# Kernel optimization log

Hardware: AMD Instinct MI355X
Metric: run time of the kernel (lower is better)

The kernel has to match this reference:

```python
import jax, jax.numpy as jnp
import numpy as np

DIM = 1024
N_HEADS = 16
HEAD_DIM = DIM // N_HEADS
HIDDEN = 4096  # round_up(4*DIM, 256)
ROPE_THETA = 10000.0
EPS = 1e-6


def setup_inputs() -> dict:
    key = jax.random.key(0)
    ks = jax.random.split(key, 10)
    s = 0.02
    return {
        "x": jax.random.normal(ks[0], (1, 4096, DIM), dtype=jnp.float32),
        "wq": jax.random.normal(ks[1], (DIM, DIM), dtype=jnp.float32) * s,
        "wk": jax.random.normal(ks[2], (DIM, DIM), dtype=jnp.float32) * s,
        "wv": jax.random.normal(ks[3], (DIM, DIM), dtype=jnp.float32) * s,
        "wo": jax.random.normal(ks[4], (DIM, DIM), dtype=jnp.float32) * s,
        "w1": jax.random.normal(ks[5], (HIDDEN, DIM), dtype=jnp.float32) * s,
        "w2": jax.random.normal(ks[6], (DIM, HIDDEN), dtype=jnp.float32) * s,
        "w3": jax.random.normal(ks[7], (HIDDEN, DIM), dtype=jnp.float32) * s,
        "g_attn": jnp.ones((DIM,), dtype=jnp.float32),
        "g_ffn": jnp.ones((DIM,), dtype=jnp.float32),
    }


def _rmsnorm(x, g):
    return x * jax.lax.rsqrt(jnp.mean(x * x, axis=-1, keepdims=True) + EPS) * g


def _rope_tables(seqlen):
    inv = 1.0 / (ROPE_THETA ** (jnp.arange(0, HEAD_DIM, 2, dtype=jnp.float32) / HEAD_DIM))
    ang = jnp.arange(seqlen, dtype=jnp.float32)[:, None] * inv[None, :]  # [s, hd/2]
    return jnp.cos(ang), jnp.sin(ang)


def _apply_rope(q, cos, sin):
    # q: [b, s, h, hd]; pairs (even, odd) treated as complex (re, im)
    b, s, h, d = q.shape
    qr = q.reshape(b, s, h, d // 2, 2)
    re, im = qr[..., 0], qr[..., 1]
    c = cos[None, :, None, :]
    sn = sin[None, :, None, :]
    out = jnp.stack([re * c - im * sn, re * sn + im * c], axis=-1)
    return out.reshape(b, s, h, d)


def reference(x, wq, wk, wv, wo, w1, w2, w3, g_attn, g_ffn):
    b, s, _ = x.shape
    xn = _rmsnorm(x, g_attn)
    q = (xn @ wq.T).reshape(b, s, N_HEADS, HEAD_DIM)
    k = (xn @ wk.T).reshape(b, s, N_HEADS, HEAD_DIM)
    v = (xn @ wv.T).reshape(b, s, N_HEADS, HEAD_DIM)
    cos, sin = _rope_tables(s)
    q = _apply_rope(q, cos, sin)
    k = _apply_rope(k, cos, sin)
    scores = jnp.einsum("bthd,bThd->bhtT", q, k) / np.sqrt(HEAD_DIM).astype(np.float32)
    probs = jax.nn.softmax(scores, axis=-1)
    attn = jnp.einsum("bhtT,bThd->bthd", probs, v).reshape(b, s, DIM)
    h = x + attn @ wo.T
    hn = _rmsnorm(h, g_ffn)
    ff = (jax.nn.silu(hn @ w1.T) * (hn @ w3.T)) @ w2.T
    return h + ff
```

## Files before the change

kernel.cpp:

```cpp
#include <hip/hip_runtime.h>

#define S_LEN 4096
#define DIMM  1024
#define NH    16
#define HD    64
#define HID   4096

typedef unsigned short u16;
typedef __attribute__((ext_vector_type(8))) short bf16x8;
typedef __attribute__((ext_vector_type(4))) short short4b;
typedef __attribute__((ext_vector_type(8))) unsigned short u16x8;
typedef __attribute__((ext_vector_type(4))) float f32x4;

__device__ __forceinline__ u16 f2bf(float f) {
  unsigned u = __float_as_uint(f);
  u += 0x7fffu + ((u >> 16) & 1u);
  return (u16)(u >> 16);
}
__device__ __forceinline__ float bf2f(u16 h) {
  return __uint_as_float(((unsigned)h) << 16);
}
__device__ __forceinline__ unsigned pack_bf16(float hi, float lo) {
  return __builtin_amdgcn_perm(__float_as_uint(hi), __float_as_uint(lo), 0x07060302u);
}
__device__ __forceinline__ float fexp2(float x) { return __builtin_amdgcn_exp2f(x); }

__device__ __forceinline__ void gl_lds16(const void* g, void* l) {
  __builtin_amdgcn_global_load_lds(
      (const __attribute__((address_space(1))) void*)g,
      (__attribute__((address_space(3))) void*)l, 16, 0, 0);
}

__global__ __launch_bounds__(256) void prep_kernel(
    const float* __restrict__ wq, const float* __restrict__ wk, const float* __restrict__ wv,
    const float* __restrict__ wo, const float* __restrict__ w1, const float* __restrict__ w3,
    const float* __restrict__ w2, const float* __restrict__ x, const float* __restrict__ g_attn,
    u16* __restrict__ wqkb, u16* __restrict__ wvb, u16* __restrict__ wob,
    u16* __restrict__ w13b, u16* __restrict__ w2b, u16* __restrict__ xnb,
    float* __restrict__ cosT, float* __restrict__ sinT) {
  int b = blockIdx.x;
  int t = threadIdx.x;
  if (b < 8192) {
    const float* src;
    u16* dst;
    int i;
    if (b < 2048) {
      int which = b >> 9, lb = b & 511;
      src = which == 0 ? wq : which == 1 ? wk : which == 2 ? wv : wo;
      dst = which == 0 ? wqkb : which == 1 ? (wqkb + (1 << 20)) : which == 2 ? wvb : wob;
      i = (lb * 256 + t) * 8;
    } else {
      int b2 = b - 2048, which = b2 >> 11, lb = b2 & 2047;
      src = which == 0 ? w1 : which == 1 ? w3 : w2;
      dst = which == 0 ? w13b : which == 1 ? (w13b + (4 << 20)) : w2b;
      i = (lb * 256 + t) * 8;
    }
    float4 a = *(const float4*)(src + i);
    float4 c = *(const float4*)(src + i + 4);
    u16x8 r;
    r[0] = f2bf(a.x); r[1] = f2bf(a.y); r[2] = f2bf(a.z); r[3] = f2bf(a.w);
    r[4] = f2bf(c.x); r[5] = f2bf(c.y); r[6] = f2bf(c.z); r[7] = f2bf(c.w);
    *(u16x8*)(dst + i) = r;
  } else if (b < 8704) {
    int idx = (b - 8192) * 256 + t;
    int pos = idx >> 5, i = idx & 31;
    double inv = pow(10000.0, -(double)(2 * i) / 64.0);
    double a = (double)pos * inv;
    cosT[idx] = (float)cos(a);
    sinT[idx] = (float)sin(a);
  } else {
    int row = b - 8704;
    const float4 v = *(const float4*)(x + (size_t)row * DIMM + t * 4);
    float ss = v.x * v.x + v.y * v.y + v.z * v.z + v.w * v.w;
#pragma unroll
    for (int off = 32; off > 0; off >>= 1) ss += __shfl_down(ss, off);
    __shared__ float red[4];
    if ((t & 63) == 0) red[t >> 6] = ss;
    __syncthreads();
    float tot = red[0] + red[1] + red[2] + red[3];
    float sc = rsqrtf(tot * (1.0f / DIMM) + 1e-6f);
    const float4 gv = *(const float4*)(g_attn + t * 4);
    ushort4 o;
    o.x = f2bf(v.x * sc * gv.x);
    o.y = f2bf(v.y * sc * gv.y);
    o.z = f2bf(v.z * sc * gv.z);
    o.w = f2bf(v.w * sc * gv.w);
    *(ushort4*)(xnb + (size_t)row * DIMM + t * 4) = o;
  }
}

__global__ __launch_bounds__(256) void rmsnorm_kernel(const float* __restrict__ x, const float* __restrict__ g,
                                                      u16* __restrict__ out) {
  int row = blockIdx.x;
  int t = threadIdx.x;
  const float4 v = *(const float4*)(x + (size_t)row * DIMM + t * 4);
  float ss = v.x * v.x + v.y * v.y + v.z * v.z + v.w * v.w;
#pragma unroll
  for (int off = 32; off > 0; off >>= 1) ss += __shfl_down(ss, off);
  __shared__ float red[4];
  if ((t & 63) == 0) red[t >> 6] = ss;
  __syncthreads();
  float tot = red[0] + red[1] + red[2] + red[3];
  float sc = rsqrtf(tot * (1.0f / DIMM) + 1e-6f);
  const float4 gv = *(const float4*)(g + t * 4);
  ushort4 o;
  o.x = f2bf(v.x * sc * gv.x);
  o.y = f2bf(v.y * sc * gv.y);
  o.z = f2bf(v.z * sc * gv.z);
  o.w = f2bf(v.w * sc * gv.w);
  *(ushort4*)(out + (size_t)row * DIMM + t * 4) = o;
}

template <int OUTMODE>
__global__ __launch_bounds__(512) void gemm_kernel(const u16* __restrict__ A, const u16* __restrict__ B,
                                                   void* Cout, const float* res, int N, int K, int lda,
                                                   int ldb, const float* cosT, const float* sinT) {
  __shared__ uint4 As0[1024], Bs0[1024], As1[1024], Bs1[1024];
  const int t = threadIdx.x;
  const int w = t >> 6, l = t & 63;
  const int wm = w >> 1, wn = w & 1;
  const int bm = blockIdx.y, bn = blockIdx.x;
  const int quad = l >> 4, lc = l & 15;

  f32x4 acc[2][4];
  const f32x4 zero = {0.0f, 0.0f, 0.0f, 0.0f};
#pragma unroll
  for (int mi = 0; mi < 2; mi++)
#pragma unroll
    for (int ni = 0; ni < 4; ni++) acc[mi][ni] = zero;

  const int band0 = t >> 6, kq0 = (t >> 4) & 3, row0 = t & 15;
  const u16* Ap0 = A + (size_t)(bm * 128 + band0 * 16 + row0) * lda + kq0 * 8;
  const u16* Bp0 = B + (size_t)(bn * 128 + band0 * 16 + row0) * ldb + kq0 * 8;
  if constexpr (OUTMODE == 4) {
    Ap0 += (size_t)blockIdx.z * K;
    Bp0 += (size_t)blockIdx.z * K;
  }
  const int abase = wm * 128 + l;
  const int bbase = wn * 256 + l;

#define STAGEL(AD, BD, K0)                 \
  do {                                     \
    gl_lds16(Ap0 + (K0), &(AD)[t]);        \
    gl_lds16(Ap0 + (K0) + 32, &(AD)[t + 512]); \
    gl_lds16(Bp0 + (K0), &(BD)[t]);        \
    gl_lds16(Bp0 + (K0) + 32, &(BD)[t + 512]); \
  } while (0)

#define COMPL(AS, BS)                                                                               \
  do {                                                                                              \
    _Pragma("unroll") for (int ks = 0; ks < 2; ks++) {                                              \
      bf16x8 af[2], bfr[4];                                                                         \
      _Pragma("unroll") for (int mi = 0; mi < 2; mi++)                                              \
          af[mi] = *(const bf16x8*)&(AS)[ks * 512 + abase + mi * 64];                               \
      _Pragma("unroll") for (int ni = 0; ni < 4; ni++)                                              \
          bfr[ni] = *(const bf16x8*)&(BS)[ks * 512 + bbase + ni * 64];                              \
      _Pragma("unroll") for (int mi = 0; mi < 2; mi++)                                              \
          _Pragma("unroll") for (int ni = 0; ni < 4; ni++)                                          \
              acc[mi][ni] = __builtin_amdgcn_mfma_f32_16x16x32_bf16(af[mi], bfr[ni], acc[mi][ni], 0, 0, 0); \
    }                                                                                               \
  } while (0)

  STAGEL(As0, Bs0, 0);
  __syncthreads();
  int k0 = 0;
  for (; k0 + 128 < K; k0 += 128) {
    STAGEL(As1, Bs1, k0 + 64);
    COMPL(As0, Bs0);
    __syncthreads();
    STAGEL(As0, Bs0, k0 + 128);
    COMPL(As1, Bs1);
    __syncthreads();
  }
  STAGEL(As1, Bs1, k0 + 64);
  COMPL(As0, Bs0);
  __syncthreads();
  COMPL(As1, Bs1);
#undef STAGEL
#undef COMPL

  const int rbase = bm * 128 + wm * 32 + quad * 4;
  const int cbase = bn * 128 + wn * 64 + lc;
  const float qs = (OUTMODE == 3 && bn < 8) ? 0.18033688011112f : 1.0f;
#pragma unroll
  for (int mi = 0; mi < 2; mi++) {
#pragma unroll
    for (int r = 0; r < 4; r++) {
      int row = rbase + mi * 16 + r;
#pragma unroll
      for (int ni = 0; ni < 4; ni++) {
        int col = cbase + ni * 16;
        if constexpr (OUTMODE == 0) {
          ((u16*)Cout)[(size_t)row * N + col] = f2bf(acc[mi][ni][r]);
        } else if constexpr (OUTMODE == 1) {
          size_t idx = (size_t)row * N + col;
          ((float*)Cout)[idx] = res[idx] + acc[mi][ni][r];
        } else if constexpr (OUTMODE == 2) {
          int h = row >> 6, din = row & 63;
          int kb = col >> 6, k63 = col & 63;
          int off = ((h << 6) + kb) * 4096 + (((din >> 4) << 1) + (k63 >> 5)) * 512 +
                    ((((k63 >> 2) & 3) << 4) + (din & 15)) * 8 + ((k63 >> 4) & 1) * 4 + (k63 & 3);
          ((u16*)Cout)[off] = f2bf(acc[mi][ni][r]);
        } else if constexpr (OUTMODE == 4) {
          size_t idx = (size_t)row * N + col;
          atomicAdd((float*)Cout + idx, acc[mi][ni][r]);
        } else {
          float v = acc[mi][ni][r];
          float pv = __shfl_xor(v, 1);
          int i = ((ni * 16 + lc) & 63) >> 1;
          float c = cosT[(row << 5) + i], s = sinT[(row << 5) + i];
          float o = (lc & 1) ? (pv * s + v * c) : (v * c - pv * s);
          ((u16*)Cout)[(size_t)row * N + col] = f2bf(o * qs);
        }
      }
    }
  }
}

__global__ __launch_bounds__(512) void gemm256_kernel(const u16* __restrict__ A, const u16* __restrict__ B,
                                                      u16* __restrict__ Cout, int N, int K, int lda) {
  __shared__ uint4 As0[1024], Bs0[1024], As1[1024], Bs1[1024], As2[1024], Bs2[1024];
  const int t = threadIdx.x;
  const int w = t >> 6, l = t & 63;
  const int wm = w >> 2, wn = w & 3;
  const int bm = blockIdx.y, bn = blockIdx.x;
  const int quad = l >> 4, lc = l & 15;

  f32x4 acc[8][4];
  const f32x4 zero = {0.0f, 0.0f, 0.0f, 0.0f};
#pragma unroll
  for (int mi = 0; mi < 8; mi++)
#pragma unroll
    for (int ni = 0; ni < 4; ni++) acc[mi][ni] = zero;

  const int band0 = t >> 6, kq0 = (t >> 4) & 3, row0 = t & 15;
  const u16* Ap0 = A + (size_t)(bm * 256 + band0 * 16 + row0) * lda + kq0 * 8;
  const u16* Bp0 = B + (size_t)(bn * 256 + band0 * 16 + row0) * K + kq0 * 8;
  const size_t Astep = (size_t)128 * lda;
  const size_t Bstep = (size_t)128 * K;

#define STG(AD, BD, K0)                           \
  do {                                            \
    gl_lds16(Ap0 + (K0), &(AD)[t]);               \
    gl_lds16(Ap0 + Astep + (K0), &(AD)[t + 512]); \
    gl_lds16(Bp0 + (K0), &(BD)[t]);               \
    gl_lds16(Bp0 + Bstep + (K0), &(BD)[t + 512]); \
  } while (0)

  const int NT = K >> 5;

#define PHASE(CA, CB, SA, SB, TT)                                              \
  do {                                                                         \
    if ((TT) + 2 < NT) STG(SA, SB, ((TT) + 2) * 32);                           \
    bf16x8 af[8], bfr[4];                                                      \
    _Pragma("unroll") for (int mi = 0; mi < 8; mi++)                           \
        af[mi] = *(const bf16x8*)&(CA)[(wm * 8 + mi) * 64 + l];                \
    _Pragma("unroll") for (int ni = 0; ni < 4; ni++)                           \
        bfr[ni] = *(const bf16x8*)&(CB)[(wn * 4 + ni) * 64 + l];               \
    __builtin_amdgcn_s_setprio(1);                                             \
    _Pragma("unroll") for (int mi = 0; mi < 8; mi++)                           \
        _Pragma("unroll") for (int ni = 0; ni < 4; ni++)                       \
            acc[mi][ni] = __builtin_amdgcn_mfma_f32_16x16x32_bf16(af[mi], bfr[ni], acc[mi][ni], 0, 0, 0); \
    __builtin_amdgcn_s_setprio(0);                                             \
    if ((TT) + 1 < NT) {                                                       \
      asm volatile("s_waitcnt lgkmcnt(0)" ::: "memory");                       \
      if ((TT) + 2 < NT) {                                                     \
        asm volatile("s_waitcnt vmcnt(4)" ::: "memory");                       \
      } else {                                                                 \
        asm volatile("s_waitcnt vmcnt(0)" ::: "memory");                       \
      }                                                                        \
      __builtin_amdgcn_s_barrier();                                            \
    }                                                                          \
  } while (0)

  STG(As0, Bs0, 0);
  STG(As1, Bs1, 32);
  asm volatile("s_waitcnt vmcnt(4)" ::: "memory");
  __builtin_amdgcn_s_barrier();

  for (int tt = 0; tt < NT; tt += 3) {
    PHASE(As0, Bs0, As2, Bs2, tt);
    if (tt + 1 < NT) PHASE(As1, Bs1, As0, Bs0, tt + 1);
    if (tt + 2 < NT) PHASE(As2, Bs2, As1, Bs1, tt + 2);
  }
#undef STG
#undef PHASE

  const int rbase = bm * 256 + wm * 128 + quad * 4;
  const int cbase = bn * 256 + wn * 64 + lc;
#pragma unroll
  for (int mi = 0; mi < 8; mi++) {
#pragma unroll
    for (int r = 0; r < 4; r++) {
      int row = rbase + mi * 16 + r;
#pragma unroll
      for (int ni = 0; ni < 4; ni++) {
        int col = cbase + ni * 16;
        Cout[(size_t)row * N + col] = f2bf(acc[mi][ni][r]);
      }
    }
  }
}

__global__ __launch_bounds__(512) void attn_kernel(const u16* __restrict__ Qm, const u16* __restrict__ Km,
                                                   const u16* __restrict__ Vsw, u16* __restrict__ Om) {
  __shared__ char smem[32768];
  uint4* Ks0 = (uint4*)smem;
  uint4* Vs0 = (uint4*)(smem + 8192);
  uint4* Ks1 = (uint4*)(smem + 16384);
  uint4* Vs1 = (uint4*)(smem + 24576);
  const int t = threadIdx.x;
  const int w = t >> 6, l = t & 63;
  const int quad = l >> 4, lc = l & 15;
  const int hd = blockIdx.y;
  const int qrow = blockIdx.x * 128 + w * 16;

  bf16x8 qf_[2];
#pragma unroll
  for (int ch = 0; ch < 2; ch++)
    qf_[ch] = *(const bf16x8*)(Qm + (size_t)(qrow + lc) * 2048 + hd * HD + ch * 32 + quad * 8);

  const f32x4 zero = {0.0f, 0.0f, 0.0f, 0.0f};
  const bf16x8 ones8 = {(short)0x3F80, (short)0x3F80, (short)0x3F80, (short)0x3F80,
                        (short)0x3F80, (short)0x3F80, (short)0x3F80, (short)0x3F80};
  f32x4 Oa[4];
#pragma unroll
  for (int df = 0; df < 4; df++) Oa[df] = zero;
  f32x4 lsacc = zero;

  const int s0 = t >> 7, c0 = (t >> 6) & 1, kq0 = (t >> 4) & 3, row0 = t & 15;
  const u16* Kp0 = Km + (size_t)(s0 * 16 + row0) * 2048 + hd * HD + c0 * 32 + kq0 * 8;
  const u16* Vp = Vsw + (size_t)(hd * HD) * 4096 + t * 8;

#define STAGEKV(KD, VD, TT)                                  \
  do {                                                       \
    gl_lds16(Kp0 + (size_t)(TT)*131072, &(KD)[t]);           \
    gl_lds16(Vp + (size_t)(TT)*4096, &(VD)[t]);              \
  } while (0)

#define TILE_COMPUTE(KS, VS)                                                                 \
  do {                                                                                       \
    f32x4 Sf[4];                                                                             \
    _Pragma("unroll") for (int kf = 0; kf < 4; kf++) {                                       \
      bf16x8 ka = *(const bf16x8*)&(KS)[kf * 128 + l];                                       \
      bf16x8 kb2 = *(const bf16x8*)&(KS)[kf * 128 + 64 + l];                                 \
      f32x4 z = __builtin_amdgcn_mfma_f32_16x16x32_bf16(ka, qf_[0], zero, 0, 0, 0);          \
      z = __builtin_amdgcn_mfma_f32_16x16x32_bf16(kb2, qf_[1], z, 0, 0, 0);                  \
      Sf[kf] = z;                                                                            \
    }                                                                                        \
    _Pragma("unroll") for (int kf = 0; kf < 4; kf++)                                         \
        _Pragma("unroll") for (int r = 0; r < 4; r++)                                        \
      Sf[kf][r] = fexp2(Sf[kf][r]);                                                          \
    union { bf16x8 v8; uint2 u2[2]; } p0, p1;                                                \
    p0.u2[0].x = pack_bf16(Sf[0][1], Sf[0][0]);                                              \
    p0.u2[0].y = pack_bf16(Sf[0][3], Sf[0][2]);                                              \
    p0.u2[1].x = pack_bf16(Sf[1][1], Sf[1][0]);                                              \
    p0.u2[1].y = pack_bf16(Sf[1][3], Sf[1][2]);                                              \
    p1.u2[0].x = pack_bf16(Sf[2][1], Sf[2][0]);                                              \
    p1.u2[0].y = pack_bf16(Sf[2][3], Sf[2][2]);                                              \
    p1.u2[1].x = pack_bf16(Sf[3][1], Sf[3][0]);                                              \
    p1.u2[1].y = pack_bf16(Sf[3][3], Sf[3][2]);                                              \
    lsacc = __builtin_amdgcn_mfma_f32_16x16x32_bf16(ones8, p0.v8, lsacc, 0, 0, 0);           \
    lsacc = __builtin_amdgcn_mfma_f32_16x16x32_bf16(ones8, p1.v8, lsacc, 0, 0, 0);           \
    _Pragma("unroll") for (int df = 0; df < 4; df++) {                                       \
      bf16x8 va = *(const bf16x8*)&(VS)[(df * 2) * 64 + l];                                  \
      bf16x8 vb = *(const bf16x8*)&(VS)[(df * 2 + 1) * 64 + l];                              \
      Oa[df] = __builtin_amdgcn_mfma_f32_16x16x32_bf16(va, p0.v8, Oa[df], 0, 0, 0);          \
      Oa[df] = __builtin_amdgcn_mfma_f32_16x16x32_bf16(vb, p1.v8, Oa[df], 0, 0, 0);          \
    }                                                                                        \
  } while (0)

  STAGEKV(Ks0, Vs0, 0);
  __syncthreads();

  for (int tt = 0; tt < 64; tt += 2) {
    STAGEKV(Ks1, Vs1, tt + 1);
    TILE_COMPUTE(Ks0, Vs0);
    __syncthreads();
    if (tt + 2 < 64) STAGEKV(Ks0, Vs0, tt + 2);
    TILE_COMPUTE(Ks1, Vs1);
    __syncthreads();
  }
#undef STAGEKV
#undef TILE_COMPUTE

  u16* ep = (u16*)smem;
  float invl = 1.0f / lsacc[0];
#pragma unroll
  for (int df = 0; df < 4; df++) {
    int qb = w * 16 + lc;
    int d = df * 16 + quad * 4;
    uint2 pv;
    pv.x = pack_bf16(Oa[df][1] * invl, Oa[df][0] * invl);
    pv.y = pack_bf16(Oa[df][3] * invl, Oa[df][2] * invl);
    *(uint2*)(ep + qb * 72 + d) = pv;
  }
  __syncthreads();
#pragma unroll
  for (int it = 0; it < 2; it++) {
    int qb = it * 64 + (t >> 3);
    int dp = (t & 7) * 8;
    u16x8 rowv = *(const u16x8*)(ep + qb * 72 + dp);
    *(u16x8*)(Om + (size_t)(blockIdx.x * 128 + qb) * DIMM + hd * HD + dp) = rowv;
  }
}

__global__ __launch_bounds__(256) void silu_mul_kernel(u16* __restrict__ u13) {
  int i = (blockIdx.x * 256 + threadIdx.x) * 8;
  int r = i >> 12, c = i & 4095;
  u16* up = u13 + (size_t)r * 8192 + c;
  u16x8 uv = *(const u16x8*)up;
  u16x8 gv = *(const u16x8*)(up + 4096);
  u16x8 o;
#pragma unroll
  for (int j = 0; j < 8; j++) {
    float a = bf2f(uv[j]);
    float b = bf2f(gv[j]);
    float sv = a / (1.0f + __expf(-a));
    o[j] = f2bf(sv * b);
  }
  *(u16x8*)up = o;
}

extern "C" void kernel_launch(void* const* d_in, const int* in_sizes, int n_in,
                              void* d_out, int out_size, void* d_ws, size_t ws_size,
                              hipStream_t stream) {
  const float* x      = (const float*)d_in[0];
  const float* wq     = (const float*)d_in[1];
  const float* wk     = (const float*)d_in[2];
  const float* wv     = (const float*)d_in[3];
  const float* wo     = (const float*)d_in[4];
  const float* w1     = (const float*)d_in[5];
  const float* w2     = (const float*)d_in[6];
  const float* w3     = (const float*)d_in[7];
  const float* g_attn = (const float*)d_in[8];
  const float* g_ffn  = (const float*)d_in[9];
  float* out = (float*)d_out;
  char* ws = (char*)d_ws;
  const size_t MB = 1ull << 20;

  u16* wqkb = (u16*)(ws + 0 * MB);
  u16* wvb  = (u16*)(ws + 4 * MB);
  u16* wob  = (u16*)(ws + 6 * MB);
  u16* w13b = (u16*)(ws + 8 * MB);
  u16* w2b  = (u16*)(ws + 24 * MB);
  u16* xnb  = (u16*)(ws + 32 * MB);
  u16* qkb  = (u16*)(ws + 40 * MB);
  u16* vswz = (u16*)(ws + 56 * MB);
  u16* attb = (u16*)(ws + 64 * MB);
  u16* u13  = (u16*)(ws + 40 * MB);
  float* cosT = (float*)(ws + 104 * MB);
  float* sinT = (float*)(ws + 104 * MB + 512 * 1024);

  prep_kernel<<<12800, 256, 0, stream>>>(wq, wk, wv, wo, w1, w3, w2, x, g_attn,
                                         wqkb, wvb, wob, w13b, w2b, xnb, cosT, sinT);

  gemm_kernel<3><<<dim3(16, 32), 512, 0, stream>>>(xnb, wqkb, qkb, nullptr, 2048, DIMM, DIMM, DIMM, cosT, sinT);
  gemm_kernel<2><<<dim3(32, 8), 512, 0, stream>>>(wvb, xnb, vswz, nullptr, S_LEN, DIMM, DIMM, DIMM, nullptr, nullptr);

  attn_kernel<<<dim3(32, 16), 512, 0, stream>>>(qkb, qkb + 1024, vswz, attb);

  gemm_kernel<1><<<dim3(8, 32), 512, 0, stream>>>(attb, wob, out, x, DIMM, DIMM, DIMM, DIMM, nullptr, nullptr);

  rmsnorm_kernel<<<4096, 256, 0, stream>>>(out, g_ffn, xnb);

  gemm256_kernel<<<dim3(32, 16), 512, 0, stream>>>(xnb, w13b, u13, 8192, DIMM, DIMM);

  silu_mul_kernel<<<8192, 256, 0, stream>>>(u13);

  gemm_kernel<4><<<dim3(8, 32, 4), 512, 0, stream>>>(u13, w2b, out, nullptr, DIMM, 1024, 8192, HID, nullptr, nullptr);
}
```

Measured before the change: 497.7 us.

## Fuse SiLU-gate multiply into W1/W3 GEMM epilogue via interleaved weight layout

Interleaves W1 and W3 rows in blocks of 1024 elements so that neighbouring output columns of the up-projection GEMM hold the matching gate and up values. The GEMM epilogue then exchanges those values between adjacent lanes, applies SiLU and the multiply, and writes a half-width bf16 result. This removes the separate silu_mul kernel and halves the intermediate written and read back. The down-projection GEMM is relaunched with a split-K of 2 over the narrower buffer. The interleave offset and the lane pairing in the epilogue have to agree for the result to be correct, and only even lanes now issue stores.

```diff
diff --git a/kernel.cpp b/kernel.cpp
--- a/kernel.cpp
+++ b/kernel.cpp
@@ -43,24 +43,32 @@
   if (b < 8192) {
     const float* src;
     u16* dst;
+    size_t o;
     int i;
     if (b < 2048) {
       int which = b >> 9, lb = b & 511;
       src = which == 0 ? wq : which == 1 ? wk : which == 2 ? wv : wo;
       dst = which == 0 ? wqkb : which == 1 ? (wqkb + (1 << 20)) : which == 2 ? wvb : wob;
       i = (lb * 256 + t) * 8;
+      o = (size_t)i;
     } else {
       int b2 = b - 2048, which = b2 >> 11, lb = b2 & 2047;
       src = which == 0 ? w1 : which == 1 ? w3 : w2;
-      dst = which == 0 ? w13b : which == 1 ? (w13b + (4 << 20)) : w2b;
       i = (lb * 256 + t) * 8;
+      if (which == 2) {
+        dst = w2b;
+        o = (size_t)i;
+      } else {
+        dst = w13b;
+        o = ((size_t)(i & ~1023) << 1) + ((size_t)which << 10) + (i & 1023);
+      }
     }
     float4 a = *(const float4*)(src + i);
     float4 c = *(const float4*)(src + i + 4);
     u16x8 r;
     r[0] = f2bf(a.x); r[1] = f2bf(a.y); r[2] = f2bf(a.z); r[3] = f2bf(a.w);
     r[4] = f2bf(c.x); r[5] = f2bf(c.y); r[6] = f2bf(c.z); r[7] = f2bf(c.w);
-    *(u16x8*)(dst + i) = r;
+    *(u16x8*)(dst + o) = r;
   } else if (b < 8704) {
     int idx = (b - 8192) * 256 + t;
     int pos = idx >> 5, i = idx & 31;
@@ -80,12 +88,12 @@
     float tot = red[0] + red[1] + red[2] + red[3];
     float sc = rsqrtf(tot * (1.0f / DIMM) + 1e-6f);
     const float4 gv = *(const float4*)(g_attn + t * 4);
-    ushort4 o;
-    o.x = f2bf(v.x * sc * gv.x);
-    o.y = f2bf(v.y * sc * gv.y);
-    o.z = f2bf(v.z * sc * gv.z);
-    o.w = f2bf(v.w * sc * gv.w);
-    *(ushort4*)(xnb + (size_t)row * DIMM + t * 4) = o;
+    ushort4 o2;
+    o2.x = f2bf(v.x * sc * gv.x);
+    o2.y = f2bf(v.y * sc * gv.y);
+    o2.z = f2bf(v.z * sc * gv.z);
+    o2.w = f2bf(v.w * sc * gv.w);
+    *(ushort4*)(xnb + (size_t)row * DIMM + t * 4) = o2;
   }
 }
 
@@ -288,6 +296,8 @@
 
   const int rbase = bm * 256 + wm * 128 + quad * 4;
   const int cbase = bn * 256 + wn * 64 + lc;
+  const int ffw = N >> 1;
+  const bool isu = (l & 1) == 0;
 #pragma unroll
   for (int mi = 0; mi < 8; mi++) {
 #pragma unroll
@@ -296,7 +306,12 @@
 #pragma unroll
       for (int ni = 0; ni < 4; ni++) {
         int col = cbase + ni * 16;
-        Cout[(size_t)row * N + col] = f2bf(acc[mi][ni][r]);
+        float v = acc[mi][ni][r];
+        float pv = __shfl_xor(v, 1);
+        if (isu) {
+          float sv = v / (1.0f + __expf(-v));
+          Cout[(size_t)row * ffw + (col >> 1)] = f2bf(sv * pv);
+        }
       }
     }
   }
@@ -405,23 +420,6 @@
   }
 }
 
-__global__ __launch_bounds__(256) void silu_mul_kernel(u16* __restrict__ u13) {
-  int i = (blockIdx.x * 256 + threadIdx.x) * 8;
-  int r = i >> 12, c = i & 4095;
-  u16* up = u13 + (size_t)r * 8192 + c;
-  u16x8 uv = *(const u16x8*)up;
-  u16x8 gv = *(const u16x8*)(up + 4096);
-  u16x8 o;
-#pragma unroll
-  for (int j = 0; j < 8; j++) {
-    float a = bf2f(uv[j]);
-    float b = bf2f(gv[j]);
-    float sv = a / (1.0f + __expf(-a));
-    o[j] = f2bf(sv * b);
-  }
-  *(u16x8*)up = o;
-}
-
 extern "C" void kernel_launch(void* const* d_in, const int* in_sizes, int n_in,
                               void* d_out, int out_size, void* d_ws, size_t ws_size,
                               hipStream_t stream) {
@@ -448,7 +446,7 @@
   u16* qkb  = (u16*)(ws + 40 * MB);
   u16* vswz = (u16*)(ws + 56 * MB);
   u16* attb = (u16*)(ws + 64 * MB);
-  u16* u13  = (u16*)(ws + 40 * MB);
+  u16* ff   = (u16*)(ws + 40 * MB);
   float* cosT = (float*)(ws + 104 * MB);
   float* sinT = (float*)(ws + 104 * MB + 512 * 1024);
 
@@ -464,9 +462,7 @@
 
   rmsnorm_kernel<<<4096, 256, 0, stream>>>(out, g_ffn, xnb);
 
-  gemm256_kernel<<<dim3(32, 16), 512, 0, stream>>>(xnb, w13b, u13, 8192, DIMM, DIMM);
-
-  silu_mul_kernel<<<8192, 256, 0, stream>>>(u13);
-
-  gemm_kernel<4><<<dim3(8, 32, 4), 512, 0, stream>>>(u13, w2b, out, nullptr, DIMM, 1024, 8192, HID, nullptr, nullptr);
-}
+  gemm256_kernel<<<dim3(32, 16), 512, 0, stream>>>(xnb, w13b, ff, 8192, DIMM, DIMM);
+
+  gemm_kernel<4><<<dim3(8, 32, 2), 512, 0, stream>>>(ff, w2b, out, nullptr, DIMM, 2048, 4096, HID, nullptr, nullptr);
+}
```

New measurement: 469.4 us. -5.7%, faster.
